# Performance work log

Hardware: AMD Instinct MI355X
Metric: run time of the kernel (lower is better)

Reference implementation:

```python
import jax, jax.numpy as jnp
import numpy as np

# dims
B, T, N, D = 4, 256, 64, 512
H, DH = 8, 64            # n_head, d_head; H*DH == D
DF = 4 * D               # SwiGLU hidden
EPS = 1e-6


def rmsnorm(x, w):
    return x * jax.lax.rsqrt(jnp.mean(x * x, axis=-1, keepdims=True) + EPS) * w


def phi(x):
    # positive feature map for kernelized (linear) attention ('SMReg' assumed elu+1 style)
    return jax.nn.elu(x) + 1.0


def heads(x):
    return x.reshape(*x.shape[:-1], H, DH)


def lin_att(Xq, Xkv, wq, wk, wv, wo):
    # low-rank high-order linear attention: kernelized attention applied
    # independently along each tensor mode (time T, entities N), averaged.
    q = phi(heads(Xq @ wq))   # [B,T,N,H,DH]
    k = phi(heads(Xkv @ wk))
    v = heads(Xkv @ wv)
    # mode 1 (time): attend over T, batch over (B,N)
    kv_t = jnp.einsum('btnhk,btnhv->bnhkv', k, v)          # [B,N,H,DH,DH]
    ks_t = k.sum(axis=1)                                   # [B,N,H,DH]
    den_t = jnp.einsum('btnhk,bnhk->btnh', q, ks_t) + EPS
    out_t = jnp.einsum('btnhk,bnhkv->btnhv', q, kv_t) / den_t[..., None]
    # mode 2 (entities): attend over N, batch over (B,T)
    kv_n = jnp.einsum('btnhk,btnhv->bthkv', k, v)
    ks_n = k.sum(axis=2)
    den_n = jnp.einsum('btnhk,bthk->btnh', q, ks_n) + EPS
    out_n = jnp.einsum('btnhk,bthkv->btnhv', q, kv_n) / den_n[..., None]
    out = 0.5 * (out_t + out_n)
    return out.reshape(*Xq.shape[:-1], H * DH) @ wo


def swiglu(x, w1, w2, w3):
    return (jax.nn.silu(x @ w1) * (x @ w3)) @ w2


def setup_inputs() -> dict:
    key = jax.random.key(0)
    ks = jax.random.split(key, 20)
    s = 0.02
    inp = {
        'X': jax.random.normal(ks[0], (B, T, N, D), jnp.float32),
        'Z': jax.random.normal(ks[1], (B, T, N, D), jnp.float32),
        'n1': jnp.ones((D,), jnp.float32),
        'n2': jnp.ones((D,), jnp.float32),
        'n3': jnp.ones((D,), jnp.float32),
        'nz': jnp.ones((D,), jnp.float32),
        'a_wq': jax.random.normal(ks[2], (D, H * DH), jnp.float32) * s,
        'a_wk': jax.random.normal(ks[3], (D, H * DH), jnp.float32) * s,
        'a_wv': jax.random.normal(ks[4], (D, H * DH), jnp.float32) * s,
        'a_wo': jax.random.normal(ks[5], (H * DH, D), jnp.float32) * s,
        'c_wq': jax.random.normal(ks[6], (D, H * DH), jnp.float32) * s,
        'c_wk': jax.random.normal(ks[7], (D, H * DH), jnp.float32) * s,
        'c_wv': jax.random.normal(ks[8], (D, H * DH), jnp.float32) * s,
        'c_wo': jax.random.normal(ks[9], (H * DH, D), jnp.float32) * s,
        'f_w1': jax.random.normal(ks[10], (D, DF), jnp.float32) * s,
        'f_w2': jax.random.normal(ks[11], (DF, D), jnp.float32) * s,
        'f_w3': jax.random.normal(ks[12], (D, DF), jnp.float32) * s,
    }
    return inp


def reference(X, Z, n1, n2, n3, nz, a_wq, a_wk, a_wv, a_wo,
              c_wq, c_wk, c_wv, c_wo, f_w1, f_w2, f_w3):
    # h = X + SelfAtt(norm1(X))
    xn = rmsnorm(X, n1)
    h = X + lin_att(xn, xn, a_wq, a_wk, a_wv, a_wo)
    # h = h + CrossAtt(norm3(h), normz(Z))
    h = h + lin_att(rmsnorm(h, n3), rmsnorm(Z, nz), c_wq, c_wk, c_wv, c_wo)
    # out = h + SwiGLU(norm2(h))   (dropout p=0 -> identity)
    return h + swiglu(rmsnorm(h, n2), f_w1, f_w2, f_w3)
```

## Files before the change

### kernel.cpp

```cpp
#include <hip/hip_runtime.h>

typedef short s16x8 __attribute__((ext_vector_type(8)));
typedef float f32x4 __attribute__((ext_vector_type(4)));
typedef unsigned short u16;
typedef unsigned int u32;

__device__ __forceinline__ float bf2f(u16 u) {
  union { unsigned int i; float f; } v; v.i = ((unsigned int)u) << 16; return v.f;
}
__device__ __forceinline__ u16 f2bf(float f) {
  union { float f; unsigned int i; } v; v.f = f;
  unsigned int r = v.i + 0x7fffu + ((v.i >> 16) & 1u);
  return (u16)(r >> 16);
}

__device__ __forceinline__ void gload16(const u16* g, u16* l) {
  __builtin_amdgcn_global_load_lds(
      (const __attribute__((address_space(1))) u32*)g,
      (__attribute__((address_space(3))) u32*)l, 16, 0, 0);
}

template<int KDIM, int NDIM>
__launch_bounds__(256)
__global__ void wprep(const float* __restrict__ in, u16* __restrict__ out) {
  __shared__ float t[64][65];
  const int tid = threadIdx.x;
  const int nb = NDIM / 64;
  const int tk0 = (blockIdx.x / nb) * 64;
  const int tn0 = (blockIdx.x % nb) * 64;
#pragma unroll
  for (int i = 0; i < 16; i++) {
    int idx = i * 256 + tid;
    int r = idx >> 6, c = idx & 63;
    t[r][c] = in[(long)(tk0 + r) * NDIM + (tn0 + c)];
  }
  __syncthreads();
#pragma unroll
  for (int i = 0; i < 16; i++) {
    int idx = i * 256 + tid;
    int nn = idx >> 6, kk = idx & 63;
    out[(long)(tn0 + nn) * KDIM + (tk0 + kk)] = f2bf(t[kk][nn]);
  }
}

__launch_bounds__(256)
__global__ void rmsnorm_f32(const float* __restrict__ x, const float* __restrict__ w,
                            u16* __restrict__ out) {
  const long row = (long)blockIdx.x * 4 + (threadIdx.x >> 6);
  const int lane = threadIdx.x & 63;
  const float* xr = x + row * 512 + lane * 8;
  float4 v0 = *(const float4*)xr;
  float4 v1 = *(const float4*)(xr + 4);
  float ss = v0.x*v0.x + v0.y*v0.y + v0.z*v0.z + v0.w*v0.w
           + v1.x*v1.x + v1.y*v1.y + v1.z*v1.z + v1.w*v1.w;
#pragma unroll
  for (int o = 1; o < 64; o <<= 1) ss += __shfl_xor(ss, o);
  float sc = rsqrtf(ss * (1.0f / 512.0f) + 1e-6f);
  const float* wp = w + lane * 8;
  float4 w0 = *(const float4*)wp;
  float4 w1 = *(const float4*)(wp + 4);
  union { u16 u[8]; uint4 v; } o;
  o.u[0] = f2bf(v0.x * sc * w0.x);
  o.u[1] = f2bf(v0.y * sc * w0.y);
  o.u[2] = f2bf(v0.z * sc * w0.z);
  o.u[3] = f2bf(v0.w * sc * w0.w);
  o.u[4] = f2bf(v1.x * sc * w1.x);
  o.u[5] = f2bf(v1.y * sc * w1.y);
  o.u[6] = f2bf(v1.z * sc * w1.z);
  o.u[7] = f2bf(v1.w * sc * w1.w);
  *(uint4*)(out + row * 512 + lane * 8) = o.v;
}

__launch_bounds__(256)
__global__ void rmsnorm_bf16(const u16* __restrict__ x, const float* __restrict__ w,
                             u16* __restrict__ out) {
  const long row = (long)blockIdx.x * 4 + (threadIdx.x >> 6);
  const int lane = threadIdx.x & 63;
  uint4 u = *(const uint4*)(x + row * 512 + lane * 8);
  const u16* us = (const u16*)&u;
  float f[8];
  float ss = 0.f;
#pragma unroll
  for (int j = 0; j < 8; j++) { f[j] = bf2f(us[j]); ss += f[j] * f[j]; }
#pragma unroll
  for (int o = 1; o < 64; o <<= 1) ss += __shfl_xor(ss, o);
  float sc = rsqrtf(ss * (1.0f / 512.0f) + 1e-6f);
  const float* wp = w + lane * 8;
  union { u16 u[8]; uint4 v; } o;
#pragma unroll
  for (int j = 0; j < 8; j++) o.u[j] = f2bf(f[j] * sc * wp[j]);
  *(uint4*)(out + row * 512 + lane * 8) = o.v;
}

enum { EPI_BF16 = 0, EPI_PHI = 1, EPI_RESX = 2, EPI_RESH = 3, EPI_SILUMUL = 4,
       EPI_OUTF = 5, EPI_QKV = 6, EPI_KV = 7 };

template<int KD, int EPI>
__launch_bounds__(512)
__global__ void gemm256(const u16* __restrict__ A, const u16* __restrict__ Bt,
                        void* __restrict__ C0, void* __restrict__ C1,
                        void* __restrict__ C2, const void* __restrict__ aux,
                        int Ns) {
  __shared__ u16 As[4][256][32];
  __shared__ u16 Bs[4][256][32];
  const int tid = threadIdx.x;
  const int lane = tid & 63;
  const int wid = tid >> 6;
  const int gx = gridDim.x;
  int L = blockIdx.y * gx + blockIdx.x;
  const int cpx = (gx * gridDim.y) >> 3;
  L = (L & 7) * cpx + (L >> 3);
  const long m0 = (long)(L / gx) * 256;
  const int nb = L % gx;
  const long n0 = (long)nb * 256;

  const int wrbase = (wid >> 2) * 128;
  const int wcbase = (wid & 3) * 64;
  const int fr = lane & 15;
  const int frq = lane >> 4;

  const int srow = lane >> 2;
  const int sslot = ((lane & 3) ^ (srow & 3)) * 8;
  const u16* Ag = A + (m0 + wid * 32 + srow) * KD + sslot;
  const u16* Bg = Bt + (n0 + wid * 32 + srow) * KD + sslot;
  u16* Al = &As[0][0][0] + wid * 1024;
  u16* Bl = &Bs[0][0][0] + wid * 1024;

  f32x4 acc[8][4] = {};

  auto STAGE = [&](int t) {
    const int b = t & 3;
    const long k0 = (long)t * 32;
    gload16(Ag + k0, Al + b * 8192);
    gload16(Ag + (long)16 * KD + k0, Al + b * 8192 + 512);
    gload16(Bg + k0, Bl + b * 8192);
    gload16(Bg + (long)16 * KD + k0, Bl + b * 8192 + 512);
  };
  auto COMPUTE = [&](int b) {
    s16x8 af[8], bf[4];
#pragma unroll
    for (int i = 0; i < 8; i++) {
      const int row = wrbase + i * 16 + fr;
      af[i] = *(const s16x8*)&As[b][row][(frq ^ (row & 3)) * 8];
    }
#pragma unroll
    for (int j = 0; j < 4; j++) {
      const int row = wcbase + j * 16 + fr;
      bf[j] = *(const s16x8*)&Bs[b][row][(frq ^ (row & 3)) * 8];
    }
    __builtin_amdgcn_s_setprio(1);
#pragma unroll
    for (int i = 0; i < 8; i++)
#pragma unroll
      for (int j = 0; j < 4; j++)
        acc[i][j] = __builtin_amdgcn_mfma_f32_16x16x32_bf16(af[i], bf[j], acc[i][j], 0, 0, 0);
    __builtin_amdgcn_s_setprio(0);
  };

  constexpr int NT = KD / 32;
  STAGE(0);
  STAGE(1);
#pragma unroll 1
  for (int t = 0; t < NT; ++t) {
    if (t + 2 < NT) {
      STAGE(t + 2);
      asm volatile("s_waitcnt vmcnt(8)" ::: "memory");
    } else if (t + 1 < NT) {
      asm volatile("s_waitcnt vmcnt(4)" ::: "memory");
    } else {
      asm volatile("s_waitcnt vmcnt(0)" ::: "memory");
    }
    __builtin_amdgcn_s_barrier();
    COMPUTE(t & 3);
    __builtin_amdgcn_s_barrier();
  }

  const int col = lane & 15;
  const int rb = frq * 4;
#pragma unroll
  for (int i = 0; i < 8; i++) {
#pragma unroll
    for (int r = 0; r < 4; r++) {
      long m = m0 + wrbase + i * 16 + rb + r;
#pragma unroll
      for (int j = 0; j < 4; j++) {
        long nlocal = wcbase + j * 16 + col;
        float v = acc[i][j][r];
        if constexpr (EPI == EPI_QKV) {
          int seg = nb >> 1;
          long off = m * 512 + ((n0 + nlocal) & 511);
          u16* P = (u16*)(seg == 0 ? C0 : (seg == 1 ? C1 : C2));
          float p = (seg < 2) ? (v > 0.f ? v + 1.f : __expf(v)) : v;
          P[off] = f2bf(p);
        } else if constexpr (EPI == EPI_KV) {
          int seg = nb >> 1;
          long off = m * 512 + ((n0 + nlocal) & 511);
          u16* P = (u16*)(seg == 0 ? C0 : C1);
          float p = (seg == 0) ? (v > 0.f ? v + 1.f : __expf(v)) : v;
          P[off] = f2bf(p);
        } else {
          long off = m * Ns + (n0 + nlocal);
          if constexpr (EPI == EPI_BF16) {
            ((u16*)C0)[off] = f2bf(v);
          } else if constexpr (EPI == EPI_PHI) {
            float p = v > 0.f ? v + 1.f : __expf(v);
            ((u16*)C0)[off] = f2bf(p);
          } else if constexpr (EPI == EPI_RESX) {
            ((u16*)C0)[off] = f2bf(((const float*)aux)[off] + v);
          } else if constexpr (EPI == EPI_RESH) {
            ((u16*)C0)[off] = f2bf(bf2f(((const u16*)aux)[off]) + v);
          } else if constexpr (EPI == EPI_SILUMUL) {
            float t2 = bf2f(((const u16*)aux)[off]);
            float s = t2 / (1.f + __expf(-t2));
            ((u16*)C0)[off] = f2bf(s * v);
          } else {
            ((float*)C0)[off] = bf2f(((const u16*)aux)[off]) + v;
          }
        }
      }
    }
  }
}

__launch_bounds__(256)
__global__ void att_mode1(const u16* __restrict__ q, const u16* __restrict__ k,
                          const u16* __restrict__ v, u16* __restrict__ attc) {
  __shared__ u16 Ks[128][72];
  __shared__ u16 Vs[128][72];
  __shared__ u16 KVT[64][72];
  __shared__ float ksump[4][64];
  __shared__ float ksum_s[64];
  __shared__ float dinv[256];
  const int tid = threadIdx.x;
  const int lane = tid & 63;
  const int w = tid >> 6;
  const int bnh = blockIdx.x;
  const int h = bnh & 7;
  const int bn = bnh >> 3;
  const int n = bn & 63;
  const int b = bn >> 6;
  const long base = ((long)b * 16384 + n) * 512 + h * 64;
  const int fr = lane & 15;
  const int fk = (lane >> 4) * 8;
  const int sdk = tid & 63, sqq = tid >> 6;

  f32x4 acc[4] = {};
  float ks_acc = 0.f;

  for (int half = 0; half < 2; half++) {
    __syncthreads();
#pragma unroll
    for (int rep = 0; rep < 4; rep++) {
      int idx = rep * 256 + tid;
      int tl = idx >> 3, c8 = idx & 7;
      long go = base + (long)(half * 128 + tl) * 32768 + c8 * 8;
      *(uint4*)&Ks[tl][c8 * 8] = *(const uint4*)(k + go);
      *(uint4*)&Vs[tl][c8 * 8] = *(const uint4*)(v + go);
    }
    __syncthreads();
#pragma unroll
    for (int i = 0; i < 32; i++) ks_acc += bf2f(Ks[sqq * 32 + i][sdk]);
#pragma unroll
    for (int ks = 0; ks < 4; ks++) {
      s16x8 af, bfr[4];
#pragma unroll
      for (int e = 0; e < 8; e++) af[e] = (short)Vs[ks * 32 + fk + e][w * 16 + fr];
#pragma unroll
      for (int j = 0; j < 4; j++)
#pragma unroll
        for (int e = 0; e < 8; e++) bfr[j][e] = (short)Ks[ks * 32 + fk + e][j * 16 + fr];
#pragma unroll
      for (int j = 0; j < 4; j++)
        acc[j] = __builtin_amdgcn_mfma_f32_16x16x32_bf16(af, bfr[j], acc[j], 0, 0, 0);
    }
  }
  ksump[sqq][sdk] = ks_acc;
  __syncthreads();
  {
    const int colL = lane & 15, rb = (lane >> 4) * 4;
#pragma unroll
    for (int j = 0; j < 4; j++)
#pragma unroll
      for (int r = 0; r < 4; r++)
        KVT[w * 16 + rb + r][j * 16 + colL] = f2bf(acc[j][r]);
  }
  if (tid < 64) ksum_s[tid] = ksump[0][tid] + ksump[1][tid] + ksump[2][tid] + ksump[3][tid];
  __syncthreads();
  {
    const u16* qp = q + base + (long)tid * 32768;
    float d = 0.f;
#pragma unroll
    for (int c8 = 0; c8 < 8; c8++) {
      uint4 u = ((const uint4*)qp)[c8];
      const u16* us = (const u16*)&u;
#pragma unroll
      for (int e = 0; e < 8; e++) d += bf2f(us[e]) * ksum_s[c8 * 8 + e];
    }
    dinv[tid] = 0.5f / (d + 1e-6f);
  }
  f32x4 acc2[4][4] = {};
#pragma unroll
  for (int ks = 0; ks < 2; ks++) {
    s16x8 aq[4], bk[4];
#pragma unroll
    for (int i = 0; i < 4; i++)
      aq[i] = *(const s16x8*)(q + base + (long)(w * 64 + i * 16 + fr) * 32768 + ks * 32 + fk);
#pragma unroll
    for (int j = 0; j < 4; j++)
      bk[j] = *(const s16x8*)&KVT[j * 16 + fr][ks * 32 + fk];
#pragma unroll
    for (int i = 0; i < 4; i++)
#pragma unroll
      for (int j = 0; j < 4; j++)
        acc2[i][j] = __builtin_amdgcn_mfma_f32_16x16x32_bf16(aq[i], bk[j], acc2[i][j], 0, 0, 0);
  }
  __syncthreads();
  const int colL = lane & 15, rb = (lane >> 4) * 4;
#pragma unroll
  for (int i = 0; i < 4; i++)
#pragma unroll
    for (int r = 0; r < 4; r++) {
      int t = w * 64 + i * 16 + rb + r;
      float inv = dinv[t];
#pragma unroll
      for (int j = 0; j < 4; j++)
        attc[base + (long)t * 32768 + j * 16 + colL] = f2bf(acc2[i][j][r] * inv);
    }
}

__launch_bounds__(256)
__global__ void att_mode2(const u16* __restrict__ q, const u16* __restrict__ k,
                          const u16* __restrict__ v, u16* __restrict__ attc) {
  __shared__ u16 Ks[64][72];
  __shared__ u16 Vs[64][72];
  __shared__ u16 KVT[64][72];
  __shared__ float ksump[4][64];
  __shared__ float ksum_s[64];
  __shared__ float dinv[64];
  const int tid = threadIdx.x;
  const int lane = tid & 63;
  const int w = tid >> 6;
  const int bth = blockIdx.x;
  const int h = bth & 7;
  const long bt = bth >> 3;
  const long base = bt * 32768 + h * 64;
  const int fr = lane & 15;
  const int fk = (lane >> 4) * 8;
  const int sdk = tid & 63, sqq = tid >> 6;

#pragma unroll
  for (int rep = 0; rep < 2; rep++) {
    int idx = rep * 256 + tid;
    int nl = idx >> 3, c8 = idx & 7;
    long go = base + (long)nl * 512 + c8 * 8;
    *(uint4*)&Ks[nl][c8 * 8] = *(const uint4*)(k + go);
    *(uint4*)&Vs[nl][c8 * 8] = *(const uint4*)(v + go);
  }
  __syncthreads();
  {
    float s = 0.f;
#pragma unroll
    for (int i = 0; i < 16; i++) s += bf2f(Ks[sqq * 16 + i][sdk]);
    ksump[sqq][sdk] = s;
  }
  f32x4 acc[4] = {};
#pragma unroll
  for (int ks = 0; ks < 2; ks++) {
    s16x8 af, bfr[4];
#pragma unroll
    for (int e = 0; e < 8; e++) af[e] = (short)Vs[ks * 32 + fk + e][w * 16 + fr];
#pragma unroll
    for (int j = 0; j < 4; j++)
#pragma unroll
      for (int e = 0; e < 8; e++) bfr[j][e] = (short)Ks[ks * 32 + fk + e][j * 16 + fr];
#pragma unroll
    for (int j = 0; j < 4; j++)
      acc[j] = __builtin_amdgcn_mfma_f32_16x16x32_bf16(af, bfr[j], acc[j], 0, 0, 0);
  }
  __syncthreads();
  {
    const int colL = lane & 15, rb = (lane >> 4) * 4;
#pragma unroll
    for (int j = 0; j < 4; j++)
#pragma unroll
      for (int r = 0; r < 4; r++)
        KVT[w * 16 + rb + r][j * 16 + colL] = f2bf(acc[j][r]);
  }
  if (tid < 64) ksum_s[tid] = ksump[0][tid] + ksump[1][tid] + ksump[2][tid] + ksump[3][tid];
  __syncthreads();
  if (tid < 64) {
    const u16* qp = q + base + (long)tid * 512;
    float d = 0.f;
#pragma unroll
    for (int c8 = 0; c8 < 8; c8++) {
      uint4 u = ((const uint4*)qp)[c8];
      const u16* us = (const u16*)&u;
#pragma unroll
      for (int e = 0; e < 8; e++) d += bf2f(us[e]) * ksum_s[c8 * 8 + e];
    }
    dinv[tid] = 0.5f / (d + 1e-6f);
  }
  f32x4 acc2[4] = {};
#pragma unroll
  for (int ks = 0; ks < 2; ks++) {
    s16x8 aq, bk[4];
    aq = *(const s16x8*)(q + base + (long)(w * 16 + fr) * 512 + ks * 32 + fk);
#pragma unroll
    for (int j = 0; j < 4; j++)
      bk[j] = *(const s16x8*)&KVT[j * 16 + fr][ks * 32 + fk];
#pragma unroll
    for (int j = 0; j < 4; j++)
      acc2[j] = __builtin_amdgcn_mfma_f32_16x16x32_bf16(aq, bk[j], acc2[j], 0, 0, 0);
  }
  __syncthreads();
  const int colL = lane & 15, rb = (lane >> 4) * 4;
#pragma unroll
  for (int r = 0; r < 4; r++) {
    int nr = w * 16 + rb + r;
    float inv = dinv[nr];
#pragma unroll
    for (int j = 0; j < 4; j++) {
      long o = base + (long)nr * 512 + j * 16 + colL;
      attc[o] = f2bf(bf2f(attc[o]) + acc2[j][r] * inv);
    }
  }
}

extern "C" void kernel_launch(void* const* d_in, const int* in_sizes, int n_in,
                              void* d_out, int out_size, void* d_ws, size_t ws_size,
                              hipStream_t stream) {
  const float* X    = (const float*)d_in[0];
  const float* Z    = (const float*)d_in[1];
  const float* n1   = (const float*)d_in[2];
  const float* n2   = (const float*)d_in[3];
  const float* n3   = (const float*)d_in[4];
  const float* nz   = (const float*)d_in[5];
  const float* a_wq = (const float*)d_in[6];
  const float* a_wk = (const float*)d_in[7];
  const float* a_wv = (const float*)d_in[8];
  const float* a_wo = (const float*)d_in[9];
  const float* c_wq = (const float*)d_in[10];
  const float* c_wk = (const float*)d_in[11];
  const float* c_wv = (const float*)d_in[12];
  const float* c_wo = (const float*)d_in[13];
  const float* f_w1 = (const float*)d_in[14];
  const float* f_w2 = (const float*)d_in[15];
  const float* f_w3 = (const float*)d_in[16];
  float* out = (float*)d_out;
  (void)ws_size; (void)in_sizes; (void)n_in; (void)out_size;

  char* p = (char*)d_ws;
  size_t off = 0;
  auto take = [&](size_t bytes) -> char* {
    char* r = p + off;
    off += (bytes + 255) & ~(size_t)255;
    return r;
  };
  u16* w_aq = (u16*)take(512 * 512 * 2);
  u16* w_ak = (u16*)take(512 * 512 * 2);
  u16* w_av = (u16*)take(512 * 512 * 2);
  u16* w_ao = (u16*)take(512 * 512 * 2);
  u16* w_cq = (u16*)take(512 * 512 * 2);
  u16* w_ck = (u16*)take(512 * 512 * 2);
  u16* w_cv = (u16*)take(512 * 512 * 2);
  u16* w_co = (u16*)take(512 * 512 * 2);
  u16* w_f1 = (u16*)take(2048 * 512 * 2);
  u16* w_f3 = (u16*)take(2048 * 512 * 2);
  u16* w_f2 = (u16*)take(512 * 2048 * 2);
  u16* xn   = (u16*)take((size_t)65536 * 512 * 2);
  u16* hbuf = (u16*)take((size_t)65536 * 512 * 2);
  u16* qbuf = (u16*)take((size_t)65536 * 512 * 2);
  u16* kbuf = (u16*)d_out;
  u16* vbuf = (u16*)d_out + (size_t)65536 * 512;
  u16* attc = xn;
  u16* tslot = qbuf;

  dim3 b256(256);
  dim3 b512(512);
  dim3 gQKV(6, 256);
  dim3 gKV(4, 256);
  dim3 gP(2, 256);
  dim3 gU(8, 64);
  dim3 gD(2, 64);

  wprep<512, 512><<<64, b256, 0, stream>>>(a_wq, w_aq);
  wprep<512, 512><<<64, b256, 0, stream>>>(a_wk, w_ak);
  wprep<512, 512><<<64, b256, 0, stream>>>(a_wv, w_av);
  wprep<512, 512><<<64, b256, 0, stream>>>(a_wo, w_ao);
  wprep<512, 512><<<64, b256, 0, stream>>>(c_wq, w_cq);
  wprep<512, 512><<<64, b256, 0, stream>>>(c_wk, w_ck);
  wprep<512, 512><<<64, b256, 0, stream>>>(c_wv, w_cv);
  wprep<512, 512><<<64, b256, 0, stream>>>(c_wo, w_co);
  wprep<512, 2048><<<256, b256, 0, stream>>>(f_w1, w_f1);
  wprep<512, 2048><<<256, b256, 0, stream>>>(f_w3, w_f3);
  wprep<2048, 512><<<256, b256, 0, stream>>>(f_w2, w_f2);

  rmsnorm_f32<<<16384, b256, 0, stream>>>(X, n1, xn);
  gemm256<512, EPI_QKV><<<gQKV, b512, 0, stream>>>(xn, w_aq, qbuf, kbuf, vbuf, nullptr, 1536);
  att_mode1<<<2048, b256, 0, stream>>>(qbuf, kbuf, vbuf, attc);
  att_mode2<<<8192, b256, 0, stream>>>(qbuf, kbuf, vbuf, attc);
  gemm256<512, EPI_RESX><<<gP, b512, 0, stream>>>(attc, w_ao, hbuf, nullptr, nullptr, X, 512);

  rmsnorm_bf16<<<16384, b256, 0, stream>>>(hbuf, n3, xn);
  gemm256<512, EPI_PHI><<<gP, b512, 0, stream>>>(xn, w_cq, qbuf, nullptr, nullptr, nullptr, 512);
  rmsnorm_f32<<<16384, b256, 0, stream>>>(Z, nz, xn);
  gemm256<512, EPI_KV><<<gKV, b512, 0, stream>>>(xn, w_ck, kbuf, vbuf, nullptr, nullptr, 1024);
  att_mode1<<<2048, b256, 0, stream>>>(qbuf, kbuf, vbuf, attc);
  att_mode2<<<8192, b256, 0, stream>>>(qbuf, kbuf, vbuf, attc);
  gemm256<512, EPI_RESH><<<gP, b512, 0, stream>>>(attc, w_co, hbuf, nullptr, nullptr, hbuf, 512);

  rmsnorm_bf16<<<16384, b256, 0, stream>>>(hbuf, n2, xn);
  const int CH = 16384;
  for (int c = 0; c < 4; c++) {
    const size_t ro = (size_t)c * CH * 512;
    gemm256<512, EPI_BF16><<<gU, b512, 0, stream>>>(xn + ro, w_f1, tslot, nullptr, nullptr, nullptr, 2048);
    gemm256<512, EPI_SILUMUL><<<gU, b512, 0, stream>>>(xn + ro, w_f3, tslot, nullptr, nullptr, tslot, 2048);
    gemm256<2048, EPI_OUTF><<<gD, b512, 0, stream>>>(tslot, w_f2, out + ro, nullptr, nullptr, hbuf + ro, 512);
  }
}
```

Before: 1.771 ms.

## Restructure GEMM mainloop into 4-phase ping-pong with 64-wide K tiles

Replaces the 4-stage, 32-wide K pipeline with a 2-buffer, 64-wide K tile. Each K tile is split into four compute phases, and each phase issues one slice of the next tile's global-to-LDS loads, so memory traffic is interleaved with MFMA work. The LDS swizzle changes to an 8-way XOR to match the wider rows, and launch bounds now request one block per SIMD set. This gives fewer but larger tiles and finer overlap of loads with compute, at the cost of more barriers per tile and a shallower prefetch depth.

```diff
diff --git a/kernel.cpp b/kernel.cpp
--- a/kernel.cpp
+++ b/kernel.cpp
@@ -96,13 +96,13 @@
        EPI_OUTF = 5, EPI_QKV = 6, EPI_KV = 7 };
 
 template<int KD, int EPI>
-__launch_bounds__(512)
-__global__ void gemm256(const u16* __restrict__ A, const u16* __restrict__ Bt,
-                        void* __restrict__ C0, void* __restrict__ C1,
-                        void* __restrict__ C2, const void* __restrict__ aux,
-                        int Ns) {
-  __shared__ u16 As[4][256][32];
-  __shared__ u16 Bs[4][256][32];
+__launch_bounds__(512, 1)
+__global__ void gemm8p(const u16* __restrict__ A, const u16* __restrict__ Bt,
+                       void* __restrict__ C0, void* __restrict__ C1,
+                       void* __restrict__ C2, const void* __restrict__ aux,
+                       int Ns) {
+  __shared__ u16 As[2][256][64];
+  __shared__ u16 Bs[2][256][64];
   const int tid = threadIdx.x;
   const int lane = tid & 63;
   const int wid = tid >> 6;
@@ -119,60 +119,61 @@
   const int fr = lane & 15;
   const int frq = lane >> 4;
 
-  const int srow = lane >> 2;
-  const int sslot = ((lane & 3) ^ (srow & 3)) * 8;
-  const u16* Ag = A + (m0 + wid * 32 + srow) * KD + sslot;
-  const u16* Bg = Bt + (n0 + wid * 32 + srow) * KD + sslot;
-  u16* Al = &As[0][0][0] + wid * 1024;
-  u16* Bl = &Bs[0][0][0] + wid * 1024;
+  const int srow8 = lane >> 3;
+  const int sg8 = ((lane & 7) ^ srow8) * 8;
+  const u16* Ag = A + (m0 + wid * 32 + srow8) * KD + sg8;
+  const u16* Bg = Bt + (n0 + wid * 32 + srow8) * KD + sg8;
 
   f32x4 acc[8][4] = {};
 
-  auto STAGE = [&](int t) {
-    const int b = t & 3;
-    const long k0 = (long)t * 32;
-    gload16(Ag + k0, Al + b * 8192);
-    gload16(Ag + (long)16 * KD + k0, Al + b * 8192 + 512);
-    gload16(Bg + k0, Bl + b * 8192);
-    gload16(Bg + (long)16 * KD + k0, Bl + b * 8192 + 512);
+  auto STAGE = [&](int t, int p) {
+    const int b = t & 1;
+    const long go = (long)p * 8 * KD + (long)t * 64;
+    gload16(Ag + go, &As[b][wid * 32 + p * 8][0]);
+    gload16(Bg + go, &Bs[b][wid * 32 + p * 8][0]);
   };
-  auto COMPUTE = [&](int b) {
-    s16x8 af[8], bf[4];
-#pragma unroll
-    for (int i = 0; i < 8; i++) {
-      const int row = wrbase + i * 16 + fr;
-      af[i] = *(const s16x8*)&As[b][row][(frq ^ (row & 3)) * 8];
-    }
-#pragma unroll
-    for (int j = 0; j < 4; j++) {
-      const int row = wcbase + j * 16 + fr;
-      bf[j] = *(const s16x8*)&Bs[b][row][(frq ^ (row & 3)) * 8];
-    }
-    __builtin_amdgcn_s_setprio(1);
-#pragma unroll
-    for (int i = 0; i < 8; i++)
-#pragma unroll
-      for (int j = 0; j < 4; j++)
-        acc[i][j] = __builtin_amdgcn_mfma_f32_16x16x32_bf16(af[i], bf[j], acc[i][j], 0, 0, 0);
-    __builtin_amdgcn_s_setprio(0);
-  };
-
-  constexpr int NT = KD / 32;
-  STAGE(0);
-  STAGE(1);
+
+  constexpr int NT = KD / 64;
+#pragma unroll
+  for (int p = 0; p < 4; p++) STAGE(0, p);
+
 #pragma unroll 1
   for (int t = 0; t < NT; ++t) {
-    if (t + 2 < NT) {
-      STAGE(t + 2);
-      asm volatile("s_waitcnt vmcnt(8)" ::: "memory");
-    } else if (t + 1 < NT) {
-      asm volatile("s_waitcnt vmcnt(4)" ::: "memory");
-    } else {
-      asm volatile("s_waitcnt vmcnt(0)" ::: "memory");
-    }
-    __builtin_amdgcn_s_barrier();
-    COMPUTE(t & 3);
-    __builtin_amdgcn_s_barrier();
+    const int rs = t & 1;
+    s16x8 bf[4];
+#pragma unroll
+    for (int ph = 0; ph < 4; ++ph) {
+      const int ih = ph & 1;
+      const int ks = ph >> 1;
+      if (t + 1 < NT) STAGE(t + 1, ph);
+      if (ph == 0) {
+        if (t + 1 < NT) asm volatile("s_waitcnt vmcnt(2)" ::: "memory");
+        else            asm volatile("s_waitcnt vmcnt(0)" ::: "memory");
+      }
+      __builtin_amdgcn_s_barrier();
+      if (ih == 0) {
+#pragma unroll
+        for (int j = 0; j < 4; j++) {
+          const int row = wcbase + j * 16 + fr;
+          bf[j] = *(const s16x8*)&Bs[rs][row][((ks * 4 + frq) ^ (fr & 7)) * 8];
+        }
+      }
+      s16x8 af[4];
+#pragma unroll
+      for (int i = 0; i < 4; i++) {
+        const int row = wrbase + (ih * 4 + i) * 16 + fr;
+        af[i] = *(const s16x8*)&As[rs][row][((ks * 4 + frq) ^ (fr & 7)) * 8];
+      }
+      __builtin_amdgcn_s_setprio(1);
+#pragma unroll
+      for (int i = 0; i < 4; i++)
+#pragma unroll
+        for (int j = 0; j < 4; j++)
+          acc[ih * 4 + i][j] =
+              __builtin_amdgcn_mfma_f32_16x16x32_bf16(af[i], bf[j], acc[ih * 4 + i][j], 0, 0, 0);
+      __builtin_amdgcn_s_setprio(0);
+      __builtin_amdgcn_s_barrier();
+    }
   }
 
   const int col = lane & 15;
@@ -496,25 +497,25 @@
   wprep<2048, 512><<<256, b256, 0, stream>>>(f_w2, w_f2);
 
   rmsnorm_f32<<<16384, b256, 0, stream>>>(X, n1, xn);
-  gemm256<512, EPI_QKV><<<gQKV, b512, 0, stream>>>(xn, w_aq, qbuf, kbuf, vbuf, nullptr, 1536);
+  gemm8p<512, EPI_QKV><<<gQKV, b512, 0, stream>>>(xn, w_aq, qbuf, kbuf, vbuf, nullptr, 1536);
   att_mode1<<<2048, b256, 0, stream>>>(qbuf, kbuf, vbuf, attc);
   att_mode2<<<8192, b256, 0, stream>>>(qbuf, kbuf, vbuf, attc);
-  gemm256<512, EPI_RESX><<<gP, b512, 0, stream>>>(attc, w_ao, hbuf, nullptr, nullptr, X, 512);
+  gemm8p<512, EPI_RESX><<<gP, b512, 0, stream>>>(attc, w_ao, hbuf, nullptr, nullptr, X, 512);
 
   rmsnorm_bf16<<<16384, b256, 0, stream>>>(hbuf, n3, xn);
-  gemm256<512, EPI_PHI><<<gP, b512, 0, stream>>>(xn, w_cq, qbuf, nullptr, nullptr, nullptr, 512);
+  gemm8p<512, EPI_PHI><<<gP, b512, 0, stream>>>(xn, w_cq, qbuf, nullptr, nullptr, nullptr, 512);
   rmsnorm_f32<<<16384, b256, 0, stream>>>(Z, nz, xn);
-  gemm256<512, EPI_KV><<<gKV, b512, 0, stream>>>(xn, w_ck, kbuf, vbuf, nullptr, nullptr, 1024);
+  gemm8p<512, EPI_KV><<<gKV, b512, 0, stream>>>(xn, w_ck, kbuf, vbuf, nullptr, nullptr, 1024);
   att_mode1<<<2048, b256, 0, stream>>>(qbuf, kbuf, vbuf, attc);
   att_mode2<<<8192, b256, 0, stream>>>(qbuf, kbuf, vbuf, attc);
-  gemm256<512, EPI_RESH><<<gP, b512, 0, stream>>>(attc, w_co, hbuf, nullptr, nullptr, hbuf, 512);
+  gemm8p<512, EPI_RESH><<<gP, b512, 0, stream>>>(attc, w_co, hbuf, nullptr, nullptr, hbuf, 512);
 
   rmsnorm_bf16<<<16384, b256, 0, stream>>>(hbuf, n2, xn);
   const int CH = 16384;
   for (int c = 0; c < 4; c++) {
     const size_t ro = (size_t)c * CH * 512;
-    gemm256<512, EPI_BF16><<<gU, b512, 0, stream>>>(xn + ro, w_f1, tslot, nullptr, nullptr, nullptr, 2048);
-    gemm256<512, EPI_SILUMUL><<<gU, b512, 0, stream>>>(xn + ro, w_f3, tslot, nullptr, nullptr, tslot, 2048);
-    gemm256<2048, EPI_OUTF><<<gD, b512, 0, stream>>>(tslot, w_f2, out + ro, nullptr, nullptr, hbuf + ro, 512);
-  }
-}
+    gemm8p<512, EPI_BF16><<<gU, b512, 0, stream>>>(xn + ro, w_f1, tslot, nullptr, nullptr, nullptr, 2048);
+    gemm8p<512, EPI_SILUMUL><<<gU, b512, 0, stream>>>(xn + ro, w_f3, tslot, nullptr, nullptr, tslot, 2048);
+    gemm8p<2048, EPI_OUTF><<<gD, b512, 0, stream>>>(tslot, w_f2, out + ro, nullptr, nullptr, hbuf + ro, 512);
+  }
+}
```

Result: slower. 1.963 ms (+10.9%).
